# Kernel tuning notes

Hardware: AMD Instinct MI355X
Metric: run time of the kernel (lower is better)

Reference implementation:

```python
import jax, jax.numpy as jnp
import numpy as np

EPS = 1e-12  # torch F.normalize eps

def _l2_normalize(x):
    n = jnp.linalg.norm(x, axis=-1, keepdims=True)
    return x / jnp.maximum(n, EPS)

def setup_inputs() -> dict:
    key = jax.random.key(0)
    k1, k2 = jax.random.split(key)
    B, F = 8192, 128
    z1 = jax.random.normal(k1, (B, F), dtype=jnp.float32)
    z2 = jax.random.normal(k2, (B, F), dtype=jnp.float32)
    return {"z1": z1, "z2": z2}

def reference(z1, z2):
    T = 1.0
    z1n = _l2_normalize(z1)
    z2n = _l2_normalize(z2)
    # Full similarity matrix S[i,j] = <z1n_i, z2n_j>.
    # Original builds logits row i = [S_ii, S_ij (j != i)], which is a
    # permutation of row i of S; CE with label 0 = logsumexp(row) - S_ii.
    S = jnp.einsum('bf,cf->bc', z1n, z2n) / T  # [B, B]
    pos = jnp.diagonal(S)                       # [B]
    lse = jax.nn.logsumexp(S, axis=1)           # [B]
    return jnp.mean(lse - pos)
```

## Files before the change

kernel.cpp:

```cpp
#include <hip/hip_runtime.h>
#include <hip/hip_bf16.h>

typedef __attribute__((ext_vector_type(8))) short bf16x8;
typedef __attribute__((ext_vector_type(4))) float f32x4;

#define B_ROWS 8192
#define FDIM 128
#define NT 8
#define BN 128
#define CHUNK (NT*BN)

#define GLOAD_LDS(gp, lp) __builtin_amdgcn_global_load_lds( \
    (const __attribute__((address_space(1))) unsigned*)(gp), \
    (__attribute__((address_space(3))) unsigned*)(lp), 16, 0, 0)

__global__ __launch_bounds__(256) void simclr_norm(const float* __restrict__ z1,
                                                   const float* __restrict__ z2,
                                                   __hip_bfloat16* __restrict__ z1n,
                                                   __hip_bfloat16* __restrict__ z2n,
                                                   float* __restrict__ pos) {
    int row  = (blockIdx.x * 256 + threadIdx.x) >> 6;
    int lane = threadIdx.x & 63;
    int c = lane * 2;
    const float2 v1 = *(const float2*)(z1 + row * FDIM + c);
    const float2 v2 = *(const float2*)(z2 + row * FDIM + c);
    float s1 = v1.x * v1.x + v1.y * v1.y;
    float s2 = v2.x * v2.x + v2.y * v2.y;
    for (int m = 32; m > 0; m >>= 1) { s1 += __shfl_xor(s1, m); s2 += __shfl_xor(s2, m); }
    float inv1 = 1.0f / fmaxf(sqrtf(s1), 1e-12f);
    float inv2 = 1.0f / fmaxf(sqrtf(s2), 1e-12f);
    float a0 = v1.x * inv1, a1 = v1.y * inv1;
    float b0 = v2.x * inv2, b1 = v2.y * inv2;
    z1n[row * FDIM + c]     = __float2bfloat16(a0);
    z1n[row * FDIM + c + 1] = __float2bfloat16(a1);
    z2n[row * FDIM + c]     = __float2bfloat16(b0);
    z2n[row * FDIM + c + 1] = __float2bfloat16(b1);
    float p = a0 * b0 + a1 * b1;
    for (int m = 32; m > 0; m >>= 1) p += __shfl_xor(p, m);
    if (lane == 0) pos[row] = p;
}

__global__ __launch_bounds__(512, 2) void simclr_gemm(const __hip_bfloat16* __restrict__ z1n,
                                                      const __hip_bfloat16* __restrict__ z2n,
                                                      float* __restrict__ rs) {
    __shared__ unsigned char smem[65536];
    const int tid = threadIdx.x;
    const int wid = tid >> 6, lane = tid & 63;
    const int lq = lane >> 4, lr = lane & 15;
    const int rowBase = blockIdx.y * 256;
    const int colBase = blockIdx.x * CHUNK;
    const int waveM = wid >> 1, waveN = wid & 1;

    const unsigned short* g1 = (const unsigned short*)z1n;
    const unsigned short* g2 = (const unsigned short*)z2n;

#pragma unroll
    for (int j = 0; j < 4; ++j) {
        int rl = wid * 16 + j * 4 + lq;
        const unsigned short* gp = g2 + (size_t)(colBase + rl) * FDIM + (lr ^ (rl & 7)) * 8;
        GLOAD_LDS(gp, smem + wid * 4096 + j * 1024);
    }

    bf16x8 a[4][4];
#pragma unroll
    for (int m = 0; m < 4; ++m) {
        int rA = rowBase + waveM * 64 + m * 16 + lr;
        const unsigned short* rp = g1 + (size_t)rA * FDIM + lq * 8;
#pragma unroll
        for (int kk = 0; kk < 4; ++kk)
            a[m][kk] = *(const bf16x8*)(rp + kk * 32);
    }

    float rowsum[4][4] = {};

    for (int t = 0; t < NT; ++t) {
        __syncthreads();
        const int cur = (t & 1) * 32768;
        if (t + 1 < NT) {
            const int colT = colBase + (t + 1) * BN;
            const int nxt = ((t + 1) & 1) * 32768;
#pragma unroll
            for (int j = 0; j < 4; ++j) {
                int rl = wid * 16 + j * 4 + lq;
                const unsigned short* gp = g2 + (size_t)(colT + rl) * FDIM + (lr ^ (rl & 7)) * 8;
                GLOAD_LDS(gp, smem + nxt + wid * 4096 + j * 1024);
            }
        }
        f32x4 acc[4][4] = {};
#pragma unroll
        for (int kk = 0; kk < 4; ++kk) {
            bf16x8 b[4];
            const int kByte = kk * 64 + lq * 16;
#pragma unroll
            for (int n = 0; n < 4; ++n) {
                int rB = waveN * 64 + n * 16 + lr;
                b[n] = *(const bf16x8*)(smem + cur + rB * 256 + (kByte ^ ((rB & 7) << 4)));
            }
#pragma unroll
            for (int m = 0; m < 4; ++m)
#pragma unroll
                for (int n = 0; n < 4; ++n)
                    acc[m][n] = __builtin_amdgcn_mfma_f32_16x16x32_bf16(a[m][kk], b[n], acc[m][n], 0, 0, 0);
        }
#pragma unroll
        for (int m = 0; m < 4; ++m)
#pragma unroll
            for (int r = 0; r < 4; ++r)
                rowsum[m][r] += __expf(acc[m][0][r]) + __expf(acc[m][1][r]) +
                                __expf(acc[m][2][r]) + __expf(acc[m][3][r]);
    }

#pragma unroll
    for (int m = 0; m < 4; ++m)
#pragma unroll
        for (int r = 0; r < 4; ++r) {
            float s = rowsum[m][r];
            s += __shfl_xor(s, 1); s += __shfl_xor(s, 2);
            s += __shfl_xor(s, 4); s += __shfl_xor(s, 8);
            if (lr == 0)
                atomicAdd(&rs[rowBase + waveM * 64 + m * 16 + lq * 4 + r], s);
        }
}

__global__ __launch_bounds__(1024) void simclr_finish(const float* __restrict__ rs,
                                                      const float* __restrict__ pos,
                                                      float* __restrict__ out) {
    __shared__ float red[16];
    int tid = threadIdx.x;
    float s = 0.0f;
    for (int i = tid; i < B_ROWS; i += 1024) s += logf(rs[i]) - pos[i];
    for (int m = 32; m > 0; m >>= 1) s += __shfl_xor(s, m);
    if ((tid & 63) == 0) red[tid >> 6] = s;
    __syncthreads();
    if (tid < 16) {
        float v = red[tid];
        for (int m = 8; m > 0; m >>= 1) v += __shfl_xor(v, m);
        if (tid == 0) *out = v / (float)B_ROWS;
    }
}

extern "C" void kernel_launch(void* const* d_in, const int* in_sizes, int n_in,
                              void* d_out, int out_size, void* d_ws, size_t ws_size,
                              hipStream_t stream) {
    const float* z1 = (const float*)d_in[0];
    const float* z2 = (const float*)d_in[1];
    float* out = (float*)d_out;
    char* ws = (char*)d_ws;

    __hip_bfloat16* z1n = (__hip_bfloat16*)ws;
    __hip_bfloat16* z2n = (__hip_bfloat16*)(ws + 2097152);
    float* pos          = (float*)(ws + 4194304);
    float* rs           = (float*)(ws + 4194304 + 32768);

    hipMemsetAsync(rs, 0, B_ROWS * sizeof(float), stream);
    simclr_norm<<<B_ROWS / 4, 256, 0, stream>>>(z1, z2, z1n, z2n, pos);
    simclr_gemm<<<dim3(NT == 8 ? 8 : 8, 32), 512, 0, stream>>>(z1n, z2n, rs);
    simclr_finish<<<1, 1024, 0, stream>>>(rs, pos, out);
}
```

Before: 42.63 us.

## Shrink GEMM tiles, fold log2e into z1n, replace atomics with partial sums

The GEMM block tile shrinks from 256x128 to 256x64 with each wave owning 32 rows, so LDS use halves and launch bounds allow 4 blocks per CU, and the grid grows to 16x32 blocks. Scaling z1n by log2(e) lets the epilogue use the hardware exp2 instead of exp. Per-row atomics into a zeroed buffer become plain stores of per-chunk partial sums, which a multi-block finish kernel reduces before applying log. The extra log2e factor rounds into bf16, and the larger grid reloads A fragments from global memory more often.

```diff
diff --git a/kernel.cpp b/kernel.cpp
--- a/kernel.cpp
+++ b/kernel.cpp
@@ -6,13 +6,21 @@
 
 #define B_ROWS 8192
 #define FDIM 128
+#define BN 64
 #define NT 8
-#define BN 128
-#define CHUNK (NT*BN)
+#define NCHUNK 16
 
 #define GLOAD_LDS(gp, lp) __builtin_amdgcn_global_load_lds( \
     (const __attribute__((address_space(1))) unsigned*)(gp), \
     (__attribute__((address_space(3))) unsigned*)(lp), 16, 0, 0)
+
+#if __has_builtin(__builtin_amdgcn_exp2f)
+#define EXP2F(x) __builtin_amdgcn_exp2f(x)
+#else
+#define EXP2F(x) exp2f(x)
+#endif
+
+#define LOG2E 1.4426950408889634f
 
 __global__ __launch_bounds__(256) void simclr_norm(const float* __restrict__ z1,
                                                    const float* __restrict__ z2,
@@ -31,8 +39,8 @@
     float inv2 = 1.0f / fmaxf(sqrtf(s2), 1e-12f);
     float a0 = v1.x * inv1, a1 = v1.y * inv1;
     float b0 = v2.x * inv2, b1 = v2.y * inv2;
-    z1n[row * FDIM + c]     = __float2bfloat16(a0);
-    z1n[row * FDIM + c + 1] = __float2bfloat16(a1);
+    z1n[row * FDIM + c]     = __float2bfloat16(a0 * LOG2E);
+    z1n[row * FDIM + c + 1] = __float2bfloat16(a1 * LOG2E);
     z2n[row * FDIM + c]     = __float2bfloat16(b0);
     z2n[row * FDIM + c + 1] = __float2bfloat16(b1);
     float p = a0 * b0 + a1 * b1;
@@ -40,102 +48,102 @@
     if (lane == 0) pos[row] = p;
 }
 
-__global__ __launch_bounds__(512, 2) void simclr_gemm(const __hip_bfloat16* __restrict__ z1n,
+__global__ __launch_bounds__(512, 4) void simclr_gemm(const __hip_bfloat16* __restrict__ z1n,
                                                       const __hip_bfloat16* __restrict__ z2n,
-                                                      float* __restrict__ rs) {
-    __shared__ unsigned char smem[65536];
+                                                      float* __restrict__ rsPart) {
+    __shared__ unsigned char smem[32768];
     const int tid = threadIdx.x;
     const int wid = tid >> 6, lane = tid & 63;
     const int lq = lane >> 4, lr = lane & 15;
     const int rowBase = blockIdx.y * 256;
-    const int colBase = blockIdx.x * CHUNK;
-    const int waveM = wid >> 1, waveN = wid & 1;
+    const int colBase = blockIdx.x * (NT * BN);
 
     const unsigned short* g1 = (const unsigned short*)z1n;
     const unsigned short* g2 = (const unsigned short*)z2n;
 
 #pragma unroll
-    for (int j = 0; j < 4; ++j) {
-        int rl = wid * 16 + j * 4 + lq;
+    for (int j = 0; j < 2; ++j) {
+        int rl = (wid * 2 + j) * 4 + lq;
         const unsigned short* gp = g2 + (size_t)(colBase + rl) * FDIM + (lr ^ (rl & 7)) * 8;
-        GLOAD_LDS(gp, smem + wid * 4096 + j * 1024);
+        GLOAD_LDS(gp, smem + wid * 2048 + j * 1024);
     }
 
-    bf16x8 a[4][4];
+    bf16x8 a[2][4];
 #pragma unroll
-    for (int m = 0; m < 4; ++m) {
-        int rA = rowBase + waveM * 64 + m * 16 + lr;
+    for (int m = 0; m < 2; ++m) {
+        int rA = rowBase + wid * 32 + m * 16 + lr;
         const unsigned short* rp = g1 + (size_t)rA * FDIM + lq * 8;
 #pragma unroll
         for (int kk = 0; kk < 4; ++kk)
             a[m][kk] = *(const bf16x8*)(rp + kk * 32);
     }
 
-    float rowsum[4][4] = {};
+    float rowsum[2][4] = {};
 
     for (int t = 0; t < NT; ++t) {
         __syncthreads();
-        const int cur = (t & 1) * 32768;
+        const int cur = (t & 1) * 16384;
         if (t + 1 < NT) {
             const int colT = colBase + (t + 1) * BN;
-            const int nxt = ((t + 1) & 1) * 32768;
+            const int nxt = ((t + 1) & 1) * 16384;
 #pragma unroll
-            for (int j = 0; j < 4; ++j) {
-                int rl = wid * 16 + j * 4 + lq;
+            for (int j = 0; j < 2; ++j) {
+                int rl = (wid * 2 + j) * 4 + lq;
                 const unsigned short* gp = g2 + (size_t)(colT + rl) * FDIM + (lr ^ (rl & 7)) * 8;
-                GLOAD_LDS(gp, smem + nxt + wid * 4096 + j * 1024);
+                GLOAD_LDS(gp, smem + nxt + wid * 2048 + j * 1024);
             }
         }
-        f32x4 acc[4][4] = {};
+        f32x4 acc[2][4] = {};
 #pragma unroll
         for (int kk = 0; kk < 4; ++kk) {
             bf16x8 b[4];
             const int kByte = kk * 64 + lq * 16;
 #pragma unroll
             for (int n = 0; n < 4; ++n) {
-                int rB = waveN * 64 + n * 16 + lr;
+                int rB = n * 16 + lr;
                 b[n] = *(const bf16x8*)(smem + cur + rB * 256 + (kByte ^ ((rB & 7) << 4)));
             }
 #pragma unroll
-            for (int m = 0; m < 4; ++m)
+            for (int m = 0; m < 2; ++m)
 #pragma unroll
                 for (int n = 0; n < 4; ++n)
                     acc[m][n] = __builtin_amdgcn_mfma_f32_16x16x32_bf16(a[m][kk], b[n], acc[m][n], 0, 0, 0);
         }
 #pragma unroll
-        for (int m = 0; m < 4; ++m)
+        for (int m = 0; m < 2; ++m)
 #pragma unroll
             for (int r = 0; r < 4; ++r)
-                rowsum[m][r] += __expf(acc[m][0][r]) + __expf(acc[m][1][r]) +
-                                __expf(acc[m][2][r]) + __expf(acc[m][3][r]);
+                rowsum[m][r] += EXP2F(acc[m][0][r]) + EXP2F(acc[m][1][r]) +
+                                EXP2F(acc[m][2][r]) + EXP2F(acc[m][3][r]);
     }
 
 #pragma unroll
-    for (int m = 0; m < 4; ++m)
+    for (int m = 0; m < 2; ++m)
 #pragma unroll
         for (int r = 0; r < 4; ++r) {
             float s = rowsum[m][r];
             s += __shfl_xor(s, 1); s += __shfl_xor(s, 2);
             s += __shfl_xor(s, 4); s += __shfl_xor(s, 8);
             if (lr == 0)
-                atomicAdd(&rs[rowBase + waveM * 64 + m * 16 + lq * 4 + r], s);
+                rsPart[blockIdx.x * B_ROWS + rowBase + wid * 32 + m * 16 + lq * 4 + r] = s;
         }
 }
 
-__global__ __launch_bounds__(1024) void simclr_finish(const float* __restrict__ rs,
-                                                      const float* __restrict__ pos,
-                                                      float* __restrict__ out) {
-    __shared__ float red[16];
-    int tid = threadIdx.x;
-    float s = 0.0f;
-    for (int i = tid; i < B_ROWS; i += 1024) s += logf(rs[i]) - pos[i];
+__global__ __launch_bounds__(256) void simclr_finish(const float* __restrict__ rsPart,
+                                                     const float* __restrict__ pos,
+                                                     float* __restrict__ out) {
+    __shared__ float red[4];
+    int i = blockIdx.x * 256 + threadIdx.x;
+    float R = 0.0f;
+#pragma unroll
+    for (int c = 0; c < NCHUNK; ++c) R += rsPart[c * B_ROWS + i];
+    float s = logf(R) - pos[i];
     for (int m = 32; m > 0; m >>= 1) s += __shfl_xor(s, m);
-    if ((tid & 63) == 0) red[tid >> 6] = s;
+    if ((threadIdx.x & 63) == 0) red[threadIdx.x >> 6] = s;
     __syncthreads();
-    if (tid < 16) {
-        float v = red[tid];
-        for (int m = 8; m > 0; m >>= 1) v += __shfl_xor(v, m);
-        if (tid == 0) *out = v / (float)B_ROWS;
+    if (threadIdx.x == 0) {
+        float v = (red[0] + red[1]) + (red[2] + red[3]);
+        atomicAdd(out, v * (1.0f / (float)B_ROWS));
     }
 }
 
@@ -150,10 +158,10 @@
     __hip_bfloat16* z1n = (__hip_bfloat16*)ws;
     __hip_bfloat16* z2n = (__hip_bfloat16*)(ws + 2097152);
     float* pos          = (float*)(ws + 4194304);
-    float* rs           = (float*)(ws + 4194304 + 32768);
+    float* rsPart       = (float*)(ws + 4194304 + 32768);
 
-    hipMemsetAsync(rs, 0, B_ROWS * sizeof(float), stream);
+    hipMemsetAsync(out, 0, sizeof(float), stream);
     simclr_norm<<<B_ROWS / 4, 256, 0, stream>>>(z1, z2, z1n, z2n, pos);
-    simclr_gemm<<<dim3(NT == 8 ? 8 : 8, 32), 512, 0, stream>>>(z1n, z2n, rs);
-    simclr_finish<<<1, 1024, 0, stream>>>(rs, pos, out);
+    simclr_gemm<<<dim3(NCHUNK, 32), 512, 0, stream>>>(z1n, z2n, rsPart);
+    simclr_finish<<<B_ROWS / 256, 256, 0, stream>>>(rsPart, pos, out);
 }
```

Measured after the change: 102.2 us. +139.8%, slower.
